# Performance work log

Measured on AMD Instinct MI355X. Metric: run time of the kernel, lower is better.

Reference implementation:

```python
import jax, jax.numpy as jnp
import numpy as np

D_MODEL = 256; D_FF = 512; D_STATE = 16; D_CONV = 4; EXPAND = 2
D_INNER = EXPAND * D_MODEL          # 512
DT_RANK = (D_MODEL + 15) // 16      # 16
BSZ = 16; NVARS = 32; PATCH_NUM = 64


def setup_inputs() -> dict:
    key = jax.random.key(0)
    ks = jax.random.split(key, 16)
    def nrm(k, shape, scale=0.02):
        return jax.random.normal(k, shape, jnp.float32) * scale
    inp = {}
    inp["x"] = jax.random.normal(ks[0], (BSZ, NVARS, D_MODEL, PATCH_NUM), jnp.float32)
    # Mamba block params
    inp["in_proj_w"] = nrm(ks[1], (2 * D_INNER, D_MODEL))
    inp["in_proj_b"] = jnp.zeros((2 * D_INNER,), jnp.float32)
    inp["conv_w"] = nrm(ks[2], (D_INNER, D_CONV), 0.1)   # depthwise causal conv
    inp["conv_b"] = jnp.zeros((D_INNER,), jnp.float32)
    inp["x_proj_w"] = nrm(ks[3], (DT_RANK + 2 * D_STATE, D_INNER))
    inp["dt_proj_w"] = nrm(ks[4], (D_INNER, DT_RANK))
    inp["dt_proj_b"] = nrm(ks[5], (D_INNER,), 0.1)
    inp["A_log"] = jnp.log(jnp.broadcast_to(
        jnp.arange(1, D_STATE + 1, dtype=jnp.float32), (D_INNER, D_STATE)))
    inp["Dp"] = jnp.ones((D_INNER,), jnp.float32)
    inp["out_proj_w"] = nrm(ks[6], (D_MODEL, D_INNER))
    # Mamba_ffn norms + pointwise FFN
    inp["norm1_g"] = jnp.ones((D_MODEL,), jnp.float32)
    inp["norm1_b"] = jnp.zeros((D_MODEL,), jnp.float32)
    inp["ffn1_w"] = nrm(ks[7], (D_FF, D_MODEL))
    inp["ffn1_b"] = jnp.zeros((D_FF,), jnp.float32)
    inp["ffn2_w"] = nrm(ks[8], (D_MODEL, D_FF))
    inp["ffn2_b"] = jnp.zeros((D_MODEL,), jnp.float32)
    inp["norm2_g"] = jnp.ones((D_MODEL,), jnp.float32)
    inp["norm2_b"] = jnp.zeros((D_MODEL,), jnp.float32)
    # outer VarPatch LayerNorm
    inp["ln_g"] = jnp.ones((D_MODEL,), jnp.float32)
    inp["ln_b"] = jnp.zeros((D_MODEL,), jnp.float32)
    return inp


def layer_norm(x, g, b, eps=1e-5):
    mu = x.mean(-1, keepdims=True)
    var = ((x - mu) ** 2).mean(-1, keepdims=True)
    return (x - mu) * jax.lax.rsqrt(var + eps) * g + b


def mamba(x, in_proj_w, in_proj_b, conv_w, conv_b, x_proj_w,
          dt_proj_w, dt_proj_b, A_log, Dp, out_proj_w):
    # x: (b, L, d_model)
    b, L, _ = x.shape
    xz = x @ in_proj_w.T + in_proj_b            # (b, L, 2*d_inner)
    xi, z = jnp.split(xz, 2, axis=-1)           # each (b, L, d_inner)
    # causal depthwise conv along L
    xc = xi.transpose(0, 2, 1)                  # (b, d_inner, L)
    xc = jax.lax.conv_general_dilated(
        xc, conv_w[:, None, :], (1,), [(D_CONV - 1, 0)],
        dimension_numbers=("NCH", "OIH", "NCH"),
        feature_group_count=D_INNER) + conv_b[None, :, None]
    xi = jax.nn.silu(xc.transpose(0, 2, 1))     # (b, L, d_inner)
    x_dbl = xi @ x_proj_w.T                     # (b, L, dt_rank + 2*n)
    dt = x_dbl[..., :DT_RANK]
    B = x_dbl[..., DT_RANK:DT_RANK + D_STATE]
    C = x_dbl[..., DT_RANK + D_STATE:]
    delta = jax.nn.softplus(dt @ dt_proj_w.T + dt_proj_b)   # (b, L, d_inner)
    A = -jnp.exp(A_log)                         # (d_inner, n)

    def step(h, inp):
        d_t, B_t, C_t, u_t = inp                # (b,d),(b,n),(b,n),(b,d)
        dA = jnp.exp(d_t[..., None] * A)        # (b, d, n)
        h = dA * h + (d_t * u_t)[..., None] * B_t[:, None, :]
        y = jnp.einsum("bdn,bn->bd", h, C_t)
        return h, y

    h0 = jnp.zeros((b, D_INNER, D_STATE), xi.dtype)
    xs = (delta.transpose(1, 0, 2), B.transpose(1, 0, 2),
          C.transpose(1, 0, 2), xi.transpose(1, 0, 2))
    _, ys = jax.lax.scan(step, h0, xs)          # ys: (L, b, d_inner)
    y = ys.transpose(1, 0, 2) + xi * Dp
    y = y * jax.nn.silu(z)
    return y @ out_proj_w.T                     # (b, L, d_model)


def reference(x, in_proj_w, in_proj_b, conv_w, conv_b, x_proj_w,
              dt_proj_w, dt_proj_b, A_log, Dp, out_proj_w,
              norm1_g, norm1_b, ffn1_w, ffn1_b, ffn2_w, ffn2_b,
              norm2_g, norm2_b, ln_g, ln_b):
    b, nv, dm, pn = x.shape
    x_residual = x
    h = x.reshape(b, pn * nv, dm)               # same flat view as torch reshape
    # Mamba_ffn: mamba + residual, norm, pointwise FFN + residual, norm
    h = h + mamba(h, in_proj_w, in_proj_b, conv_w, conv_b, x_proj_w,
                  dt_proj_w, dt_proj_b, A_log, Dp, out_proj_w)
    h = layer_norm(h, norm1_g, norm1_b)
    y = jax.nn.relu(h @ ffn1_w.T + ffn1_b)      # 1x1 conv == linear
    y = y @ ffn2_w.T + ffn2_b
    h = layer_norm(h + y, norm2_g, norm2_b)
    # back to patches
    h = h.reshape(b, nv, pn, dm)
    h = layer_norm(h, ln_g, ln_b).transpose(0, 1, 3, 2)   # (b, nv, dm, pn)
    return h + x_residual
```

## Files before the change

### kernel.cpp

```cpp
#include <hip/hip_runtime.h>
#include <hip/hip_bf16.h>
#include <math.h>

#define SEQ    2048
#define NBTOT  16
#define NCH    64
#define CHL    32

#define L2E 1.4426950408889634f

typedef __attribute__((ext_vector_type(8))) __bf16 bf16x8;
typedef __attribute__((ext_vector_type(4))) float f32x4;
typedef __attribute__((ext_vector_type(2))) float f32x2;

#define GLOAD16(gp, lp)                                                   \
  __builtin_amdgcn_global_load_lds(                                       \
      (const __attribute__((address_space(1))) unsigned int*)(gp),        \
      (__attribute__((address_space(3))) unsigned int*)(lp), 16, 0, 0)

__device__ __forceinline__ float exp2_(float x) {
  return __builtin_amdgcn_exp2f(x);
}
__device__ __forceinline__ float silu_(float x) {
  return x * __builtin_amdgcn_rcpf(1.f + exp2_(-x * L2E));
}
__device__ __forceinline__ float softplus_(float x) {
  return fmaxf(x, 0.f) + __logf(1.f + exp2_(-fabsf(x) * L2E));
}
__device__ __forceinline__ float wsum_(float v) {
#pragma unroll
  for (int off = 32; off > 0; off >>= 1) v += __shfl_xor(v, off, 64);
  return v;
}
__device__ __forceinline__ int xcdswz_(int bid, int nwg) {
  return (bid & 7) * (nwg >> 3) + (bid >> 3);
}
__device__ __forceinline__ void powpairs_(float e1, f32x2 p[8]) {
  float e2 = e1 * e1;
  f32x2 p0; p0.x = e1; p0.y = e2;
  f32x2 s2; s2.x = e2; s2.y = e2;
  f32x2 s4 = s2 * s2;
  f32x2 s8 = s4 * s4;
  p[0] = p0;      p[1] = p0 * s2; p[2] = p0 * s4; p[3] = p[1] * s4;
  p[4] = p0 * s8; p[5] = p[1] * s8; p[6] = p[2] * s8; p[7] = p[3] * s8;
}

template <bool BIAS, bool RELU, bool RES, bool RESB, bool F32OUT, bool BF16OUT,
          int NTLOG>
__global__ __launch_bounds__(256) void gemm_bf16(
    const __hip_bfloat16* __restrict__ A, const __hip_bfloat16* __restrict__ W,
    const float* __restrict__ bias, const float* __restrict__ res,
    const __hip_bfloat16* __restrict__ resb, float* __restrict__ C,
    __hip_bfloat16* __restrict__ Cb, int N, int K) {
  __shared__ __align__(16) char ShRaw[36864];
  short* Als = reinterpret_cast<short*>(ShRaw);
  short* Bls = Als + 8192;
  const int tid = threadIdx.x;
  const int lane = tid & 63;
  const int wid = tid >> 6;
  const int swz = xcdswz_(blockIdx.x, gridDim.x);
  const int m0 = (swz >> NTLOG) * 128;
  const int n0 = (swz & ((1 << NTLOG) - 1)) * 128;
  const int wm = (wid >> 1) * 64;
  const int wn = (wid & 1) * 64;
  const int lr = lane & 15;
  const int lk = lane >> 4;

  f32x4 acc[4][4];
#pragma unroll
  for (int m = 0; m < 4; ++m)
#pragma unroll
    for (int n = 0; n < 4; ++n) acc[m][n] = (f32x4){0.f, 0.f, 0.f, 0.f};

  const int srow = wid * 32 + (lane >> 3);
  const int scol = (lane & 7) * 8;
  const __hip_bfloat16* Ag = A + (size_t)(m0 + srow) * K + scol;
  const __hip_bfloat16* Wg = W + (size_t)(n0 + srow) * K + scol;
  short* Alb = Als + wid * 2048;
  short* Blb = Bls + wid * 2048;

  for (int kt = 0; kt < K; kt += 64) {
#pragma unroll
    for (int i = 0; i < 4; ++i) {
      GLOAD16(Ag + (size_t)(i * 8) * K + kt, Alb + i * 512);
      GLOAD16(Wg + (size_t)(i * 8) * K + kt, Blb + i * 512);
    }
    __syncthreads();
    const bf16x8* Af = reinterpret_cast<const bf16x8*>(Als);
    const bf16x8* Bf = reinterpret_cast<const bf16x8*>(Bls);
#pragma unroll
    for (int ks = 0; ks < 2; ++ks) {
      bf16x8 av[4], bv[4];
#pragma unroll
      for (int m = 0; m < 4; ++m)
        av[m] = Af[(wm + m * 16 + lr) * 8 + ks * 4 + lk];
#pragma unroll
      for (int n = 0; n < 4; ++n)
        bv[n] = Bf[(wn + n * 16 + lr) * 8 + ks * 4 + lk];
#pragma unroll
      for (int m = 0; m < 4; ++m)
#pragma unroll
        for (int n = 0; n < 4; ++n)
          acc[m][n] = __builtin_amdgcn_mfma_f32_16x16x32_bf16(
              av[m], bv[n], acc[m][n], 0, 0, 0);
    }
    __syncthreads();
  }

  if (BF16OUT) {
    __hip_bfloat16* epi =
        reinterpret_cast<__hip_bfloat16*>(ShRaw) + wid * 4608;
#pragma unroll
    for (int n = 0; n < 4; ++n) {
      int col = n0 + wn + n * 16 + lr;
      float bval = BIAS ? bias[col] : 0.f;
#pragma unroll
      for (int m = 0; m < 4; ++m) {
        int lrow = m * 16 + lk * 4;
#pragma unroll
        for (int r = 0; r < 4; ++r) {
          float v = acc[m][n][r];
          if (BIAS) v += bval;
          if (RES) v += res[(size_t)(m0 + wm + lrow + r) * N + col];
          if (RESB)
            v += __bfloat162float(resb[(size_t)(m0 + wm + lrow + r) * N + col]);
          if (RELU) v = fmaxf(v, 0.f);
          epi[(lrow + r) * 72 + n * 16 + lr] = __float2bfloat16(v);
        }
      }
    }
    const int lr8 = (lane & 7) * 8;
    const int lrw = lane >> 3;
    const size_t obase = (size_t)(m0 + wm) * N + n0 + wn + lr8;
#pragma unroll
    for (int j = 0; j < 8; ++j) {
      int row = j * 8 + lrw;
      int4 vv = *reinterpret_cast<const int4*>(epi + row * 72 + lr8);
      *reinterpret_cast<int4*>(&Cb[obase + (size_t)row * N]) = vv;
    }
  }
  if (F32OUT) {
#pragma unroll
    for (int n = 0; n < 4; ++n) {
      int col = n0 + wn + n * 16 + lr;
      if (col >= N) continue;
      float bval = BIAS ? bias[col] : 0.f;
#pragma unroll
      for (int m = 0; m < 4; ++m) {
        int row0 = m0 + wm + m * 16 + lk * 4;
#pragma unroll
        for (int r = 0; r < 4; ++r) {
          size_t off = (size_t)(row0 + r) * N + col;
          float v = acc[m][n][r];
          if (BIAS) v += bval;
          if (RES) v += res[off];
          if (RESB) v += __bfloat162float(resb[off]);
          if (RELU) v = fmaxf(v, 0.f);
          C[off] = v;
        }
      }
    }
  }
}

__global__ __launch_bounds__(256) void cast_bf16_k(
    const float* __restrict__ src, __hip_bfloat16* __restrict__ dst, int n4) {
  int i = xcdswz_(blockIdx.x, gridDim.x) * 256 + threadIdx.x;
  if (i >= n4) return;
  float4 v = reinterpret_cast<const float4*>(src)[i];
  union { __hip_bfloat16 h[4]; short4 s4; } u;
  u.h[0] = __float2bfloat16(v.x); u.h[1] = __float2bfloat16(v.y);
  u.h[2] = __float2bfloat16(v.z); u.h[3] = __float2bfloat16(v.w);
  reinterpret_cast<short4*>(dst)[i] = u.s4;
}

__global__ __launch_bounds__(256) void pad_wx_k(
    const float* __restrict__ src, __hip_bfloat16* __restrict__ dst) {
  int i = blockIdx.x * 256 + threadIdx.x;
  int row = i >> 7;
  union { __hip_bfloat16 h[4]; short4 s4; } u;
  if (row < 48) {
    float4 v = reinterpret_cast<const float4*>(src)[i];
    u.h[0] = __float2bfloat16(v.x); u.h[1] = __float2bfloat16(v.y);
    u.h[2] = __float2bfloat16(v.z); u.h[3] = __float2bfloat16(v.w);
  } else {
    u.h[0] = u.h[1] = u.h[2] = u.h[3] = __float2bfloat16(0.f);
  }
  reinterpret_cast<short4*>(dst)[i] = u.s4;
}

__global__ __launch_bounds__(256) void conv_silu_k(
    const __hip_bfloat16* __restrict__ xz, const float* __restrict__ cw,
    const float* __restrict__ cb, __hip_bfloat16* __restrict__ xi) {
  int idx = xcdswz_(blockIdx.x, gridDim.x) * 256 + threadIdx.x;
  int t = idx & 63;
  int rp = idx >> 6;
  int r = rp << 1;
  int l = r & (SEQ - 1);
  int c8 = t << 3;
  const __hip_bfloat16* p = xz + (size_t)r * 1024 + c8;
  union U8 { int4 v; __hip_bfloat16 h[8]; } x0, x1, x2, x3, x4, oa, ob;
  const int4 z4 = make_int4(0, 0, 0, 0);
  x4.v = *reinterpret_cast<const int4*>(p + 1024);
  x3.v = *reinterpret_cast<const int4*>(p);
  x2.v = (l >= 1) ? *reinterpret_cast<const int4*>(p - 1024) : z4;
  x1.v = (l >= 2) ? *reinterpret_cast<const int4*>(p - 2048) : z4;
  x0.v = (l >= 3) ? *reinterpret_cast<const int4*>(p - 3072) : z4;
  const float4* cw4 = reinterpret_cast<const float4*>(cw);
#pragma unroll
  for (int j = 0; j < 8; ++j) {
    float4 w = cw4[c8 + j];
    float b = cb[c8 + j];
    float f0 = __bfloat162float(x0.h[j]);
    float f1 = __bfloat162float(x1.h[j]);
    float f2 = __bfloat162float(x2.h[j]);
    float f3 = __bfloat162float(x3.h[j]);
    float f4 = __bfloat162float(x4.h[j]);
    float a0 = fmaf(w.w, f3, fmaf(w.z, f2, fmaf(w.y, f1, fmaf(w.x, f0, b))));
    float a1 = fmaf(w.w, f4, fmaf(w.z, f3, fmaf(w.y, f2, fmaf(w.x, f1, b))));
    oa.h[j] = __float2bfloat16(silu_(a0));
    ob.h[j] = __float2bfloat16(silu_(a1));
  }
  *reinterpret_cast<int4*>(&xi[(size_t)r * 512 + c8]) = oa.v;
  *reinterpret_cast<int4*>(&xi[(size_t)(r + 1) * 512 + c8]) = ob.v;
}

__global__ __launch_bounds__(256) void scan_p1(
    const __hip_bfloat16* __restrict__ u, const float* __restrict__ xdbl,
    const float* __restrict__ A_log, const float* __restrict__ wdt,
    const float* __restrict__ bdt, float* __restrict__ dlsum,
    __hip_bfloat16* __restrict__ hp, __hip_bfloat16* __restrict__ deltab) {
  const int w = xcdswz_(blockIdx.x, gridDim.x);
  const int b = w >> 7;
  const int c = (w >> 1) & 63;
  const int d = ((w & 1) << 8) + threadIdx.x;
  const int l0 = c * CHL;
  float A2[16];
  f32x2 w2[8];
  {
    const float4* aq = reinterpret_cast<const float4*>(&A_log[d * 16]);
    const f32x2* wq = reinterpret_cast<const f32x2*>(&wdt[d * 16]);
#pragma unroll
    for (int q = 0; q < 4; ++q) {
      float4 v = aq[q];
      A2[q * 4 + 0] = -exp2_(v.x * L2E) * L2E;
      A2[q * 4 + 1] = -exp2_(v.y * L2E) * L2E;
      A2[q * 4 + 2] = -exp2_(v.z * L2E) * L2E;
      A2[q * 4 + 3] = -exp2_(v.w * L2E) * L2E;
    }
#pragma unroll
    for (int k = 0; k < 8; ++k) w2[k] = wq[k];
  }
  bool chainok = true;
#pragma unroll
  for (int n = 1; n < 16; ++n)
    chainok = chainok &&
              (fabsf(A2[n] - (float)(n + 1) * A2[0]) <=
               1e-4f * (float)(n + 1) * fabsf(A2[0]));
  const float bdtd = bdt[d];
  const float nL = A2[0];
  f32x2 h2[8];
#pragma unroll
  for (int k = 0; k < 8; ++k) h2[k] = (f32x2){0.f, 0.f};
  float dls = 0.f;
  size_t base = (size_t)(b * SEQ + l0) * 512 + d;
  const float* rowp = xdbl + (size_t)(b * SEQ + l0) * 48;
  if (chainok) {
#pragma unroll 4
    for (int i = 0; i < CHL; ++i) {
      const f32x2* r2 = reinterpret_cast<const f32x2*>(rowp + i * 48);
      f32x2 acc2; acc2.x = bdtd; acc2.y = 0.f;
#pragma unroll
      for (int k = 0; k < 8; ++k)
        acc2 = __builtin_elementwise_fma(r2[k], w2[k], acc2);
      float dl = softplus_(acc2.x + acc2.y);
      deltab[base + (size_t)i * 512] = __float2bfloat16(dl);
      dls += dl;
      float du = dl * __bfloat162float(u[base + (size_t)i * 512]);
      f32x2 p[8];
      powpairs_(exp2_(dl * nL), p);
      f32x2 du2; du2.x = du; du2.y = du;
#pragma unroll
      for (int k = 0; k < 8; ++k)
        h2[k] = __builtin_elementwise_fma(p[k], h2[k], du2 * r2[8 + k]);
    }
  } else {
#pragma unroll 2
    for (int i = 0; i < CHL; ++i) {
      const f32x2* r2 = reinterpret_cast<const f32x2*>(rowp + i * 48);
      f32x2 acc2; acc2.x = bdtd; acc2.y = 0.f;
#pragma unroll
      for (int k = 0; k < 8; ++k)
        acc2 = __builtin_elementwise_fma(r2[k], w2[k], acc2);
      float dl = softplus_(acc2.x + acc2.y);
      deltab[base + (size_t)i * 512] = __float2bfloat16(dl);
      dls += dl;
      float du = dl * __bfloat162float(u[base + (size_t)i * 512]);
      f32x2 du2; du2.x = du; du2.y = du;
#pragma unroll
      for (int k = 0; k < 8; ++k) {
        f32x2 a; a.x = exp2_(dl * A2[2 * k]); a.y = exp2_(dl * A2[2 * k + 1]);
        h2[k] = __builtin_elementwise_fma(a, h2[k], du2 * r2[8 + k]);
      }
    }
  }
  size_t sc = (size_t)(b * NCH + c) * 512 + d;
  dlsum[sc] = dls;
  union { __hip_bfloat16 h[4]; short4 s4; } o0, o1, o2, o3;
#pragma unroll
  for (int j = 0; j < 2; ++j) {
    o0.h[2*j] = __float2bfloat16(h2[j].x);   o0.h[2*j+1] = __float2bfloat16(h2[j].y);
    o1.h[2*j] = __float2bfloat16(h2[2+j].x); o1.h[2*j+1] = __float2bfloat16(h2[2+j].y);
    o2.h[2*j] = __float2bfloat16(h2[4+j].x); o2.h[2*j+1] = __float2bfloat16(h2[4+j].y);
    o3.h[2*j] = __float2bfloat16(h2[6+j].x); o3.h[2*j+1] = __float2bfloat16(h2[6+j].y);
  }
  short4* hq = reinterpret_cast<short4*>(hp + sc * 16);
  hq[0] = o0.s4; hq[1] = o1.s4; hq[2] = o2.s4; hq[3] = o3.s4;
}

__global__ __launch_bounds__(256) void scan_p2(
    __hip_bfloat16* hp, const float* __restrict__ dlsum,
    const float* __restrict__ A_log) {
  int g = xcdswz_(blockIdx.x, gridDim.x) * 256 + threadIdx.x;
  int b = g >> 13;
  int dn = g & 8191;
  int d = dn >> 4;
  float A2n = -exp2_(A_log[dn] * L2E) * L2E;
  float H = 0.f;
  for (int c = 0; c < NCH; ++c) {
    float ds = dlsum[(size_t)(b * NCH + c) * 512 + d];
    size_t idx = (size_t)(b * NCH + c) * 8192 + dn;
    float p = __bfloat162float(hp[idx]);
    float a = exp2_(A2n * ds);
    hp[idx] = __float2bfloat16(H);
    H = fmaf(a, H, p);
  }
}

__global__ __launch_bounds__(256) void scan_p3(
    const __hip_bfloat16* u,
    const float* __restrict__ A_log,
    const __hip_bfloat16* __restrict__ deltab, const float* __restrict__ xdbl,
    const __hip_bfloat16* __restrict__ Hc, const float* __restrict__ Dp,
    const __hip_bfloat16* __restrict__ xz, __hip_bfloat16* y) {
  const int w = xcdswz_(blockIdx.x, gridDim.x);
  const int b = w >> 7;
  const int c = (w >> 1) & 63;
  const int d = ((w & 1) << 8) + threadIdx.x;
  const int l0 = c * CHL;
  float A2[16];
  {
    const float4* aq = reinterpret_cast<const float4*>(&A_log[d * 16]);
#pragma unroll
    for (int q = 0; q < 4; ++q) {
      float4 v = aq[q];
      A2[q * 4 + 0] = -exp2_(v.x * L2E) * L2E;
      A2[q * 4 + 1] = -exp2_(v.y * L2E) * L2E;
      A2[q * 4 + 2] = -exp2_(v.z * L2E) * L2E;
      A2[q * 4 + 3] = -exp2_(v.w * L2E) * L2E;
    }
  }
  bool chainok = true;
#pragma unroll
  for (int n = 1; n < 16; ++n)
    chainok = chainok &&
              (fabsf(A2[n] - (float)(n + 1) * A2[0]) <=
               1e-4f * (float)(n + 1) * fabsf(A2[0]));
  const float nL = A2[0];
  f32x2 h2[8];
  {
    const short4* hq =
        reinterpret_cast<const short4*>(Hc + ((size_t)(b * NCH + c) * 512 + d) * 16);
#pragma unroll
    for (int q = 0; q < 4; ++q) {
      union { short4 s4; __hip_bfloat16 h[4]; } iv;
      iv.s4 = hq[q];
      h2[2*q].x = __bfloat162float(iv.h[0]);
      h2[2*q].y = __bfloat162float(iv.h[1]);
      h2[2*q+1].x = __bfloat162float(iv.h[2]);
      h2[2*q+1].y = __bfloat162float(iv.h[3]);
    }
  }
  const float Dpd = Dp[d];
  size_t base = (size_t)(b * SEQ + l0) * 512 + d;
  const float* rowp = xdbl + (size_t)(b * SEQ + l0) * 48;
  const __hip_bfloat16* zp = xz + (size_t)(b * SEQ + l0) * 1024 + 512 + d;
  if (chainok) {
#pragma unroll 4
    for (int i = 0; i < CHL; ++i) {
      const f32x2* r2 = reinterpret_cast<const f32x2*>(rowp + i * 48);
      float dl = __bfloat162float(deltab[base + (size_t)i * 512]);
      float ul = __bfloat162float(u[base + (size_t)i * 512]);
      float du = dl * ul;
      f32x2 p[8];
      powpairs_(exp2_(dl * nL), p);
      f32x2 du2; du2.x = du; du2.y = du;
      f32x2 yv2; yv2.x = 0.f; yv2.y = 0.f;
#pragma unroll
      for (int k = 0; k < 8; ++k) {
        h2[k] = __builtin_elementwise_fma(p[k], h2[k], du2 * r2[8 + k]);
        yv2 = __builtin_elementwise_fma(h2[k], r2[16 + k], yv2);
      }
      float yv = yv2.x + yv2.y;
      float zv = __bfloat162float(zp[(size_t)i * 1024]);
      y[base + (size_t)i * 512] =
          __float2bfloat16((yv + ul * Dpd) * silu_(zv));
    }
  } else {
#pragma unroll 2
    for (int i = 0; i < CHL; ++i) {
      const f32x2* r2 = reinterpret_cast<const f32x2*>(rowp + i * 48);
      float dl = __bfloat162float(deltab[base + (size_t)i * 512]);
      float ul = __bfloat162float(u[base + (size_t)i * 512]);
      float du = dl * ul;
      f32x2 du2; du2.x = du; du2.y = du;
      f32x2 yv2; yv2.x = 0.f; yv2.y = 0.f;
#pragma unroll
      for (int k = 0; k < 8; ++k) {
        f32x2 a; a.x = exp2_(dl * A2[2 * k]); a.y = exp2_(dl * A2[2 * k + 1]);
        h2[k] = __builtin_elementwise_fma(a, h2[k], du2 * r2[8 + k]);
        yv2 = __builtin_elementwise_fma(h2[k], r2[16 + k], yv2);
      }
      float yv = yv2.x + yv2.y;
      float zv = __bfloat162float(zp[(size_t)i * 1024]);
      y[base + (size_t)i * 512] =
          __float2bfloat16((yv + ul * Dpd) * silu_(zv));
    }
  }
}

__global__ __launch_bounds__(256) void ln_k(
    const __hip_bfloat16* __restrict__ in, const float* __restrict__ g,
    const float* __restrict__ bb, __hip_bfloat16* __restrict__ outb) {
  int row = (xcdswz_(blockIdx.x, gridDim.x) * 256 + threadIdx.x) >> 6;
  int lane = threadIdx.x & 63;
  union { short4 s4; __hip_bfloat16 h[4]; } iv;
  iv.s4 = reinterpret_cast<const short4*>(in)[row * 64 + lane];
  float v0 = __bfloat162float(iv.h[0]), v1 = __bfloat162float(iv.h[1]);
  float v2 = __bfloat162float(iv.h[2]), v3 = __bfloat162float(iv.h[3]);
  float mu = wsum_(v0 + v1 + v2 + v3) * (1.f / 256.f);
  float a0 = v0 - mu, a1 = v1 - mu, a2 = v2 - mu, a3 = v3 - mu;
  float var = wsum_(a0 * a0 + a1 * a1 + a2 * a2 + a3 * a3) * (1.f / 256.f);
  float rs = __builtin_amdgcn_rsqf(var + 1e-5f);
  float4 gg = *reinterpret_cast<const float4*>(&g[lane * 4]);
  float4 bq = *reinterpret_cast<const float4*>(&bb[lane * 4]);
  union { __hip_bfloat16 h[4]; short4 s4; } u;
  u.h[0] = __float2bfloat16(a0 * rs * gg.x + bq.x);
  u.h[1] = __float2bfloat16(a1 * rs * gg.y + bq.y);
  u.h[2] = __float2bfloat16(a2 * rs * gg.z + bq.z);
  u.h[3] = __float2bfloat16(a3 * rs * gg.w + bq.w);
  reinterpret_cast<short4*>(outb)[row * 64 + lane] = u.s4;
}

__global__ __launch_bounds__(256) void final_k(
    const __hip_bfloat16* __restrict__ t2, const float* __restrict__ g2v,
    const float* __restrict__ b2v, const float* __restrict__ g3v,
    const float* __restrict__ b3v, const float* __restrict__ x,
    float* __restrict__ out) {
  int bx = xcdswz_(blockIdx.x, gridDim.x);
  int half = bx & 1, nv = (bx >> 1) & 31, b = bx >> 6;
  int wave = threadIdx.x >> 6, lane = threadIdx.x & 63;
  __shared__ float sh[32][257];
  float4 gg2 = *reinterpret_cast<const float4*>(&g2v[lane * 4]);
  float4 bb2 = *reinterpret_cast<const float4*>(&b2v[lane * 4]);
  float4 gg3 = *reinterpret_cast<const float4*>(&g3v[lane * 4]);
  float4 bb3 = *reinterpret_cast<const float4*>(&b3v[lane * 4]);
#pragma unroll
  for (int i = 0; i < 8; ++i) {
    int pn = wave * 8 + i;
    int r = ((b * 32 + nv) << 6) + (half << 5) + pn;
    union { short4 s4; __hip_bfloat16 h[4]; } iv;
    iv.s4 = reinterpret_cast<const short4*>(t2)[r * 64 + lane];
    float v0 = __bfloat162float(iv.h[0]), v1 = __bfloat162float(iv.h[1]);
    float v2 = __bfloat162float(iv.h[2]), v3 = __bfloat162float(iv.h[3]);
    float mu = wsum_(v0 + v1 + v2 + v3) * (1.f / 256.f);
    float a0 = v0 - mu, a1 = v1 - mu, a2 = v2 - mu, a3 = v3 - mu;
    float var = wsum_(a0 * a0 + a1 * a1 + a2 * a2 + a3 * a3) * (1.f / 256.f);
    float rs = __builtin_amdgcn_rsqf(var + 1e-5f);
    a0 = a0 * rs * gg2.x + bb2.x; a1 = a1 * rs * gg2.y + bb2.y;
    a2 = a2 * rs * gg2.z + bb2.z; a3 = a3 * rs * gg2.w + bb2.w;
    mu = wsum_(a0 + a1 + a2 + a3) * (1.f / 256.f);
    float c0 = a0 - mu, c1 = a1 - mu, c2 = a2 - mu, c3 = a3 - mu;
    var = wsum_(c0 * c0 + c1 * c1 + c2 * c2 + c3 * c3) * (1.f / 256.f);
    rs = __builtin_amdgcn_rsqf(var + 1e-5f);
    sh[pn][lane * 4 + 0] = c0 * rs * gg3.x + bb3.x;
    sh[pn][lane * 4 + 1] = c1 * rs * gg3.y + bb3.y;
    sh[pn][lane * 4 + 2] = c2 * rs * gg3.z + bb3.z;
    sh[pn][lane * 4 + 3] = c3 * rs * gg3.w + bb3.w;
  }
  __syncthreads();
  int pnl = threadIdx.x & 31;
  int dbase = threadIdx.x >> 5;
  size_t obase = (size_t)((b * 32 + nv) * 256) * 64 + (half << 5) + pnl;
#pragma unroll
  for (int k = 0; k < 32; ++k) {
    int dd = dbase + (k << 3);
    size_t oi = obase + (size_t)dd * 64;
    out[oi] = sh[pnl][dd] + x[oi];
  }
}

extern "C" void kernel_launch(void* const* d_in, const int* in_sizes, int n_in,
                              void* d_out, int out_size, void* d_ws,
                              size_t ws_size, hipStream_t stream) {
  const float* x    = (const float*)d_in[0];
  const float* w_in = (const float*)d_in[1];
  const float* b_in = (const float*)d_in[2];
  const float* cw   = (const float*)d_in[3];
  const float* cb   = (const float*)d_in[4];
  const float* wx   = (const float*)d_in[5];
  const float* wdt  = (const float*)d_in[6];
  const float* bdt  = (const float*)d_in[7];
  const float* alog = (const float*)d_in[8];
  const float* Dp   = (const float*)d_in[9];
  const float* wout = (const float*)d_in[10];
  const float* g1   = (const float*)d_in[11];
  const float* b1   = (const float*)d_in[12];
  const float* wf1  = (const float*)d_in[13];
  const float* bf1  = (const float*)d_in[14];
  const float* wf2  = (const float*)d_in[15];
  const float* bf2  = (const float*)d_in[16];
  const float* g2   = (const float*)d_in[17];
  const float* b2   = (const float*)d_in[18];
  const float* g3   = (const float*)d_in[19];
  const float* b3   = (const float*)d_in[20];
  float* out = (float*)d_out;

  const size_t MB1 = 1048576;
  char* g = (char*)d_ws;
  __hip_bfloat16* wbf_in  = (__hip_bfloat16*)(g);
  __hip_bfloat16* wbf_out = (__hip_bfloat16*)(g + 524288);
  __hip_bfloat16* wbf_f1  = (__hip_bfloat16*)(g + 786432);
  __hip_bfloat16* wbf_f2  = (__hip_bfloat16*)(g + 1048576);
  __hip_bfloat16* wbf_xp  = (__hip_bfloat16*)(g + 1310720);
  const size_t SHARED = 1572864;

  const size_t PB = 11 * MB1 + 393216;
  int nb = (int)((ws_size - SHARED) / PB);
  if (ws_size <= SHARED || nb < 1) return;
  if (nb > NBTOT) nb = NBTOT;

  dim3 blk(256);
  cast_bf16_k<<<dim3(256), blk, 0, stream>>>(w_in, wbf_in, 65536);
  cast_bf16_k<<<dim3(128), blk, 0, stream>>>(wout, wbf_out, 32768);
  cast_bf16_k<<<dim3(128), blk, 0, stream>>>(wf1, wbf_f1, 32768);
  cast_bf16_k<<<dim3(128), blk, 0, stream>>>(wf2, wbf_f2, 32768);
  pad_wx_k<<<dim3(64), blk, 0, stream>>>(wx, wbf_xp);

  for (int b0 = 0; b0 < NBTOT; b0 += nb) {
    int bn = (NBTOT - b0 < nb) ? (NBTOT - b0) : nb;
    char* base = g + SHARED;
    char* RA = base;
    char* RB = base + (size_t)bn * 4 * MB1;
    char* RC = base + (size_t)bn * 5 * MB1;
    char* RD = base + (size_t)bn * 7 * MB1;
    char* RE = RD + (size_t)bn * 393216;
    char* RF = RE + (size_t)bn * 2 * MB1;

    __hip_bfloat16* xz     = (__hip_bfloat16*)RA;
    __hip_bfloat16* t2b    = (__hip_bfloat16*)RA;
    __hip_bfloat16* xbf    = (__hip_bfloat16*)RB;
    float*          dlsum  = (float*)RB;
    __hip_bfloat16* xibf   = (__hip_bfloat16*)RC;
    __hip_bfloat16* ffnybf = (__hip_bfloat16*)RC;
    float*          xdbl   = (float*)RD;
    __hip_bfloat16* hp     = (__hip_bfloat16*)RE;
    __hip_bfloat16* resb   = (__hip_bfloat16*)RE;
    __hip_bfloat16* h1bf   = (__hip_bfloat16*)(RE + (size_t)bn * MB1);
    __hip_bfloat16* deltab = (__hip_bfloat16*)RF;

    const float* xg = x + (size_t)b0 * SEQ * 256;
    float* outg = out + (size_t)b0 * SEQ * 256;
    int M = bn * SEQ;
    int MT = M / 128;

    cast_bf16_k<<<dim3(M * 64 / 256), blk, 0, stream>>>(xg, xbf, M * 64);
    gemm_bf16<true, false, false, false, false, true, 3>
        <<<dim3(8 * MT), blk, 0, stream>>>(xbf, wbf_in, b_in, nullptr, nullptr,
                                           nullptr, xz, 1024, 256);
    conv_silu_k<<<dim3(M / 8), blk, 0, stream>>>(xz, cw, cb, xibf);
    gemm_bf16<false, false, false, false, true, false, 0>
        <<<dim3(MT), blk, 0, stream>>>(xibf, wbf_xp, nullptr, nullptr,
                                       nullptr, xdbl, nullptr, 48, 512);
    scan_p1<<<dim3(bn * 128), blk, 0, stream>>>(xibf, xdbl, alog, wdt, bdt,
                                                dlsum, hp, deltab);
    scan_p2<<<dim3(bn * 32), blk, 0, stream>>>(hp, dlsum, alog);
    scan_p3<<<dim3(bn * 128), blk, 0, stream>>>(xibf, alog, deltab, xdbl,
                                                hp, Dp, xz, xibf);
    gemm_bf16<false, false, true, false, false, true, 1>
        <<<dim3(2 * MT), blk, 0, stream>>>(xibf, wbf_out, nullptr, xg, nullptr,
                                           nullptr, resb, 256, 512);
    ln_k<<<dim3(M / 4), blk, 0, stream>>>(resb, g1, b1, h1bf);
    gemm_bf16<true, true, false, false, false, true, 2>
        <<<dim3(4 * MT), blk, 0, stream>>>(h1bf, wbf_f1, bf1, nullptr, nullptr,
                                           nullptr, ffnybf, 512, 256);
    gemm_bf16<true, false, false, true, false, true, 1>
        <<<dim3(2 * MT), blk, 0, stream>>>(ffnybf, wbf_f2, bf2, nullptr, h1bf,
                                           nullptr, t2b, 256, 512);
    final_k<<<dim3(bn * 64), blk, 0, stream>>>(t2b, g2, b2, g3, b3, xg, outg);
  }
}
```

Baseline: 260.5 us.

## Process two scan chunks per thread and read residuals from bf16 input copy

scan_p1 and scan_p3 now have each thread handle two adjacent chunks, interleaved in one loop. This halves the grid and gives more independent work per thread to hide exp and memory latency. Separately, the out_proj residual and the final residual add now read the bf16 copy of x instead of the fp32 input. That cuts global traffic but adds rounding error to the residual, and dlsum moves to its own buffer so xbf is not overwritten. Using bf16 x for the final residual may reduce output accuracy.

Result: slower. 266.4 us (+2.2%).

```diff
diff --git a/kernel.cpp b/kernel.cpp
--- a/kernel.cpp
+++ b/kernel.cpp
@@ -231,10 +231,10 @@
     const float* __restrict__ bdt, float* __restrict__ dlsum,
     __hip_bfloat16* __restrict__ hp, __hip_bfloat16* __restrict__ deltab) {
   const int w = xcdswz_(blockIdx.x, gridDim.x);
-  const int b = w >> 7;
-  const int c = (w >> 1) & 63;
+  const int b = w >> 6;
+  const int ch = (w >> 1) & 31;
   const int d = ((w & 1) << 8) + threadIdx.x;
-  const int l0 = c * CHL;
+  const int ca = ch * 2, cb_ = ch * 2 + 1;
   float A2[16];
   f32x2 w2[8];
   {
@@ -259,63 +259,92 @@
                1e-4f * (float)(n + 1) * fabsf(A2[0]));
   const float bdtd = bdt[d];
   const float nL = A2[0];
-  f32x2 h2[8];
-#pragma unroll
-  for (int k = 0; k < 8; ++k) h2[k] = (f32x2){0.f, 0.f};
-  float dls = 0.f;
-  size_t base = (size_t)(b * SEQ + l0) * 512 + d;
-  const float* rowp = xdbl + (size_t)(b * SEQ + l0) * 48;
+  f32x2 h2a[8], h2b[8];
+#pragma unroll
+  for (int k = 0; k < 8; ++k) {
+    h2a[k] = (f32x2){0.f, 0.f};
+    h2b[k] = (f32x2){0.f, 0.f};
+  }
+  float dlsa = 0.f, dlsb = 0.f;
+  size_t basea = (size_t)(b * SEQ + ca * CHL) * 512 + d;
+  size_t baseb = (size_t)(b * SEQ + cb_ * CHL) * 512 + d;
+  const float* rowpa = xdbl + (size_t)(b * SEQ + ca * CHL) * 48;
+  const float* rowpb = xdbl + (size_t)(b * SEQ + cb_ * CHL) * 48;
   if (chainok) {
-#pragma unroll 4
-    for (int i = 0; i < CHL; ++i) {
-      const f32x2* r2 = reinterpret_cast<const f32x2*>(rowp + i * 48);
-      f32x2 acc2; acc2.x = bdtd; acc2.y = 0.f;
-#pragma unroll
-      for (int k = 0; k < 8; ++k)
-        acc2 = __builtin_elementwise_fma(r2[k], w2[k], acc2);
-      float dl = softplus_(acc2.x + acc2.y);
-      deltab[base + (size_t)i * 512] = __float2bfloat16(dl);
-      dls += dl;
-      float du = dl * __bfloat162float(u[base + (size_t)i * 512]);
-      f32x2 p[8];
-      powpairs_(exp2_(dl * nL), p);
-      f32x2 du2; du2.x = du; du2.y = du;
-#pragma unroll
-      for (int k = 0; k < 8; ++k)
-        h2[k] = __builtin_elementwise_fma(p[k], h2[k], du2 * r2[8 + k]);
-    }
-  } else {
 #pragma unroll 2
     for (int i = 0; i < CHL; ++i) {
-      const f32x2* r2 = reinterpret_cast<const f32x2*>(rowp + i * 48);
-      f32x2 acc2; acc2.x = bdtd; acc2.y = 0.f;
-#pragma unroll
-      for (int k = 0; k < 8; ++k)
-        acc2 = __builtin_elementwise_fma(r2[k], w2[k], acc2);
-      float dl = softplus_(acc2.x + acc2.y);
-      deltab[base + (size_t)i * 512] = __float2bfloat16(dl);
-      dls += dl;
-      float du = dl * __bfloat162float(u[base + (size_t)i * 512]);
-      f32x2 du2; du2.x = du; du2.y = du;
+      const f32x2* ra = reinterpret_cast<const f32x2*>(rowpa + i * 48);
+      const f32x2* rb = reinterpret_cast<const f32x2*>(rowpb + i * 48);
+      f32x2 da; da.x = bdtd; da.y = 0.f;
+      f32x2 db; db.x = bdtd; db.y = 0.f;
 #pragma unroll
       for (int k = 0; k < 8; ++k) {
-        f32x2 a; a.x = exp2_(dl * A2[2 * k]); a.y = exp2_(dl * A2[2 * k + 1]);
-        h2[k] = __builtin_elementwise_fma(a, h2[k], du2 * r2[8 + k]);
+        da = __builtin_elementwise_fma(ra[k], w2[k], da);
+        db = __builtin_elementwise_fma(rb[k], w2[k], db);
       }
-    }
-  }
-  size_t sc = (size_t)(b * NCH + c) * 512 + d;
-  dlsum[sc] = dls;
-  union { __hip_bfloat16 h[4]; short4 s4; } o0, o1, o2, o3;
-#pragma unroll
-  for (int j = 0; j < 2; ++j) {
-    o0.h[2*j] = __float2bfloat16(h2[j].x);   o0.h[2*j+1] = __float2bfloat16(h2[j].y);
-    o1.h[2*j] = __float2bfloat16(h2[2+j].x); o1.h[2*j+1] = __float2bfloat16(h2[2+j].y);
-    o2.h[2*j] = __float2bfloat16(h2[4+j].x); o2.h[2*j+1] = __float2bfloat16(h2[4+j].y);
-    o3.h[2*j] = __float2bfloat16(h2[6+j].x); o3.h[2*j+1] = __float2bfloat16(h2[6+j].y);
-  }
-  short4* hq = reinterpret_cast<short4*>(hp + sc * 16);
-  hq[0] = o0.s4; hq[1] = o1.s4; hq[2] = o2.s4; hq[3] = o3.s4;
+      float dla = softplus_(da.x + da.y);
+      float dlb = softplus_(db.x + db.y);
+      deltab[basea + (size_t)i * 512] = __float2bfloat16(dla);
+      deltab[baseb + (size_t)i * 512] = __float2bfloat16(dlb);
+      dlsa += dla; dlsb += dlb;
+      float dua = dla * __bfloat162float(u[basea + (size_t)i * 512]);
+      float dub = dlb * __bfloat162float(u[baseb + (size_t)i * 512]);
+      f32x2 pa[8], pb[8];
+      powpairs_(exp2_(dla * nL), pa);
+      powpairs_(exp2_(dlb * nL), pb);
+      f32x2 dua2; dua2.x = dua; dua2.y = dua;
+      f32x2 dub2; dub2.x = dub; dub2.y = dub;
+#pragma unroll
+      for (int k = 0; k < 8; ++k) {
+        h2a[k] = __builtin_elementwise_fma(pa[k], h2a[k], dua2 * ra[8 + k]);
+        h2b[k] = __builtin_elementwise_fma(pb[k], h2b[k], dub2 * rb[8 + k]);
+      }
+    }
+  } else {
+#pragma unroll 1
+    for (int pass = 0; pass < 2; ++pass) {
+      size_t base = pass ? baseb : basea;
+      const float* rowp = pass ? rowpb : rowpa;
+      f32x2* h2 = pass ? h2b : h2a;
+      float dls = 0.f;
+      for (int i = 0; i < CHL; ++i) {
+        const f32x2* r2 = reinterpret_cast<const f32x2*>(rowp + i * 48);
+        f32x2 acc2; acc2.x = bdtd; acc2.y = 0.f;
+#pragma unroll
+        for (int k = 0; k < 8; ++k)
+          acc2 = __builtin_elementwise_fma(r2[k], w2[k], acc2);
+        float dl = softplus_(acc2.x + acc2.y);
+        deltab[base + (size_t)i * 512] = __float2bfloat16(dl);
+        dls += dl;
+        float du = dl * __bfloat162float(u[base + (size_t)i * 512]);
+        f32x2 du2; du2.x = du; du2.y = du;
+#pragma unroll
+        for (int k = 0; k < 8; ++k) {
+          f32x2 a; a.x = exp2_(dl * A2[2 * k]); a.y = exp2_(dl * A2[2 * k + 1]);
+          h2[k] = __builtin_elementwise_fma(a, h2[k], du2 * r2[8 + k]);
+        }
+      }
+      if (pass) dlsb = dls; else dlsa = dls;
+    }
+  }
+  size_t sca = (size_t)(b * NCH + ca) * 512 + d;
+  size_t scb = (size_t)(b * NCH + cb_) * 512 + d;
+  dlsum[sca] = dlsa;
+  dlsum[scb] = dlsb;
+#pragma unroll
+  for (int pass = 0; pass < 2; ++pass) {
+    const f32x2* h2 = pass ? h2b : h2a;
+    short4* hq = reinterpret_cast<short4*>(hp + (pass ? scb : sca) * 16);
+#pragma unroll
+    for (int q = 0; q < 4; ++q) {
+      union { __hip_bfloat16 h[4]; short4 s4; } o;
+      o.h[0] = __float2bfloat16(h2[2 * q].x);
+      o.h[1] = __float2bfloat16(h2[2 * q].y);
+      o.h[2] = __float2bfloat16(h2[2 * q + 1].x);
+      o.h[3] = __float2bfloat16(h2[2 * q + 1].y);
+      hq[q] = o.s4;
+    }
+  }
 }
 
 __global__ __launch_bounds__(256) void scan_p2(
@@ -344,10 +373,10 @@
     const __hip_bfloat16* __restrict__ Hc, const float* __restrict__ Dp,
     const __hip_bfloat16* __restrict__ xz, __hip_bfloat16* y) {
   const int w = xcdswz_(blockIdx.x, gridDim.x);
-  const int b = w >> 7;
-  const int c = (w >> 1) & 63;
+  const int b = w >> 6;
+  const int ch = (w >> 1) & 31;
   const int d = ((w & 1) << 8) + threadIdx.x;
-  const int l0 = c * CHL;
+  const int ca = ch * 2, cb_ = ch * 2 + 1;
   float A2[16];
   {
     const float4* aq = reinterpret_cast<const float4*>(&A_log[d * 16]);
@@ -367,64 +396,89 @@
               (fabsf(A2[n] - (float)(n + 1) * A2[0]) <=
                1e-4f * (float)(n + 1) * fabsf(A2[0]));
   const float nL = A2[0];
-  f32x2 h2[8];
+  f32x2 h2a[8], h2b[8];
   {
-    const short4* hq =
-        reinterpret_cast<const short4*>(Hc + ((size_t)(b * NCH + c) * 512 + d) * 16);
+    const short4* hqa =
+        reinterpret_cast<const short4*>(Hc + ((size_t)(b * NCH + ca) * 512 + d) * 16);
+    const short4* hqb =
+        reinterpret_cast<const short4*>(Hc + ((size_t)(b * NCH + cb_) * 512 + d) * 16);
 #pragma unroll
     for (int q = 0; q < 4; ++q) {
-      union { short4 s4; __hip_bfloat16 h[4]; } iv;
-      iv.s4 = hq[q];
-      h2[2*q].x = __bfloat162float(iv.h[0]);
-      h2[2*q].y = __bfloat162float(iv.h[1]);
-      h2[2*q+1].x = __bfloat162float(iv.h[2]);
-      h2[2*q+1].y = __bfloat162float(iv.h[3]);
+      union { short4 s4; __hip_bfloat16 h[4]; } ia, ib;
+      ia.s4 = hqa[q]; ib.s4 = hqb[q];
+      h2a[2*q].x = __bfloat162float(ia.h[0]);
+      h2a[2*q].y = __bfloat162float(ia.h[1]);
+      h2a[2*q+1].x = __bfloat162float(ia.h[2]);
+      h2a[2*q+1].y = __bfloat162float(ia.h[3]);
+      h2b[2*q].x = __bfloat162float(ib.h[0]);
+      h2b[2*q].y = __bfloat162float(ib.h[1]);
+      h2b[2*q+1].x = __bfloat162float(ib.h[2]);
+      h2b[2*q+1].y = __bfloat162float(ib.h[3]);
     }
   }
   const float Dpd = Dp[d];
-  size_t base = (size_t)(b * SEQ + l0) * 512 + d;
-  const float* rowp = xdbl + (size_t)(b * SEQ + l0) * 48;
-  const __hip_bfloat16* zp = xz + (size_t)(b * SEQ + l0) * 1024 + 512 + d;
+  size_t basea = (size_t)(b * SEQ + ca * CHL) * 512 + d;
+  size_t baseb = (size_t)(b * SEQ + cb_ * CHL) * 512 + d;
+  const float* rowpa = xdbl + (size_t)(b * SEQ + ca * CHL) * 48;
+  const float* rowpb = xdbl + (size_t)(b * SEQ + cb_ * CHL) * 48;
+  const __hip_bfloat16* zpa = xz + (size_t)(b * SEQ + ca * CHL) * 1024 + 512 + d;
+  const __hip_bfloat16* zpb = xz + (size_t)(b * SEQ + cb_ * CHL) * 1024 + 512 + d;
   if (chainok) {
-#pragma unroll 4
-    for (int i = 0; i < CHL; ++i) {
-      const f32x2* r2 = reinterpret_cast<const f32x2*>(rowp + i * 48);
-      float dl = __bfloat162float(deltab[base + (size_t)i * 512]);
-      float ul = __bfloat162float(u[base + (size_t)i * 512]);
-      float du = dl * ul;
-      f32x2 p[8];
-      powpairs_(exp2_(dl * nL), p);
-      f32x2 du2; du2.x = du; du2.y = du;
-      f32x2 yv2; yv2.x = 0.f; yv2.y = 0.f;
-#pragma unroll
-      for (int k = 0; k < 8; ++k) {
-        h2[k] = __builtin_elementwise_fma(p[k], h2[k], du2 * r2[8 + k]);
-        yv2 = __builtin_elementwise_fma(h2[k], r2[16 + k], yv2);
-      }
-      float yv = yv2.x + yv2.y;
-      float zv = __bfloat162float(zp[(size_t)i * 1024]);
-      y[base + (size_t)i * 512] =
-          __float2bfloat16((yv + ul * Dpd) * silu_(zv));
-    }
-  } else {
 #pragma unroll 2
     for (int i = 0; i < CHL; ++i) {
-      const f32x2* r2 = reinterpret_cast<const f32x2*>(rowp + i * 48);
-      float dl = __bfloat162float(deltab[base + (size_t)i * 512]);
-      float ul = __bfloat162float(u[base + (size_t)i * 512]);
-      float du = dl * ul;
-      f32x2 du2; du2.x = du; du2.y = du;
-      f32x2 yv2; yv2.x = 0.f; yv2.y = 0.f;
+      const f32x2* ra = reinterpret_cast<const f32x2*>(rowpa + i * 48);
+      const f32x2* rb = reinterpret_cast<const f32x2*>(rowpb + i * 48);
+      float dla = __bfloat162float(deltab[basea + (size_t)i * 512]);
+      float dlb = __bfloat162float(deltab[baseb + (size_t)i * 512]);
+      float ula = __bfloat162float(u[basea + (size_t)i * 512]);
+      float ulb = __bfloat162float(u[baseb + (size_t)i * 512]);
+      float dua = dla * ula, dub = dlb * ulb;
+      f32x2 pa[8], pb[8];
+      powpairs_(exp2_(dla * nL), pa);
+      powpairs_(exp2_(dlb * nL), pb);
+      f32x2 dua2; dua2.x = dua; dua2.y = dua;
+      f32x2 dub2; dub2.x = dub; dub2.y = dub;
+      f32x2 ya2; ya2.x = 0.f; ya2.y = 0.f;
+      f32x2 yb2; yb2.x = 0.f; yb2.y = 0.f;
 #pragma unroll
       for (int k = 0; k < 8; ++k) {
-        f32x2 a; a.x = exp2_(dl * A2[2 * k]); a.y = exp2_(dl * A2[2 * k + 1]);
-        h2[k] = __builtin_elementwise_fma(a, h2[k], du2 * r2[8 + k]);
-        yv2 = __builtin_elementwise_fma(h2[k], r2[16 + k], yv2);
+        h2a[k] = __builtin_elementwise_fma(pa[k], h2a[k], dua2 * ra[8 + k]);
+        h2b[k] = __builtin_elementwise_fma(pb[k], h2b[k], dub2 * rb[8 + k]);
+        ya2 = __builtin_elementwise_fma(h2a[k], ra[16 + k], ya2);
+        yb2 = __builtin_elementwise_fma(h2b[k], rb[16 + k], yb2);
       }
-      float yv = yv2.x + yv2.y;
-      float zv = __bfloat162float(zp[(size_t)i * 1024]);
-      y[base + (size_t)i * 512] =
-          __float2bfloat16((yv + ul * Dpd) * silu_(zv));
+      float yva = ya2.x + ya2.y + ula * Dpd;
+      float yvb = yb2.x + yb2.y + ulb * Dpd;
+      float zva = __bfloat162float(zpa[(size_t)i * 1024]);
+      float zvb = __bfloat162float(zpb[(size_t)i * 1024]);
+      y[basea + (size_t)i * 512] = __float2bfloat16(yva * silu_(zva));
+      y[baseb + (size_t)i * 512] = __float2bfloat16(yvb * silu_(zvb));
+    }
+  } else {
+#pragma unroll 1
+    for (int pass = 0; pass < 2; ++pass) {
+      size_t base = pass ? baseb : basea;
+      const float* rowp = pass ? rowpb : rowpa;
+      const __hip_bfloat16* zp = pass ? zpb : zpa;
+      f32x2* h2 = pass ? h2b : h2a;
+      for (int i = 0; i < CHL; ++i) {
+        const f32x2* r2 = reinterpret_cast<const f32x2*>(rowp + i * 48);
+        float dl = __bfloat162float(deltab[base + (size_t)i * 512]);
+        float ul = __bfloat162float(u[base + (size_t)i * 512]);
+        float du = dl * ul;
+        f32x2 du2; du2.x = du; du2.y = du;
+        f32x2 yv2; yv2.x = 0.f; yv2.y = 0.f;
+#pragma unroll
+        for (int k = 0; k < 8; ++k) {
+          f32x2 a; a.x = exp2_(dl * A2[2*k]); a.y = exp2_(dl * A2[2*k+1]);
+          h2[k] = __builtin_elementwise_fma(a, h2[k], du2 * r2[8 + k]);
+          yv2 = __builtin_elementwise_fma(h2[k], r2[16 + k], yv2);
+        }
+        float yv = yv2.x + yv2.y;
+        float zv = __bfloat162float(zp[(size_t)i * 1024]);
+        y[base + (size_t)i * 512] =
+            __float2bfloat16((yv + ul * Dpd) * silu_(zv));
+      }
     }
   }
 }
@@ -455,7 +509,7 @@
 __global__ __launch_bounds__(256) void final_k(
     const __hip_bfloat16* __restrict__ t2, const float* __restrict__ g2v,
     const float* __restrict__ b2v, const float* __restrict__ g3v,
-    const float* __restrict__ b3v, const float* __restrict__ x,
+    const float* __restrict__ b3v, const __hip_bfloat16* __restrict__ xbf,
     float* __restrict__ out) {
   int bx = xcdswz_(blockIdx.x, gridDim.x);
   int half = bx & 1, nv = (bx >> 1) & 31, b = bx >> 6;
@@ -496,7 +550,7 @@
   for (int k = 0; k < 32; ++k) {
     int dd = dbase + (k << 3);
     size_t oi = obase + (size_t)dd * 64;
-    out[oi] = sh[pnl][dd] + x[oi];
+    out[oi] = sh[pnl][dd] + __bfloat162float(xbf[oi]);
   }
 }
 
@@ -535,7 +589,7 @@
   __hip_bfloat16* wbf_xp  = (__hip_bfloat16*)(g + 1310720);
   const size_t SHARED = 1572864;
 
-  const size_t PB = 11 * MB1 + 393216;
+  const size_t PB = 11 * MB1 + 393216 + 131072;
   int nb = (int)((ws_size - SHARED) / PB);
   if (ws_size <= SHARED || nb < 1) return;
   if (nb > NBTOT) nb = NBTOT;
@@ -556,11 +610,11 @@
     char* RD = base + (size_t)bn * 7 * MB1;
     char* RE = RD + (size_t)bn * 393216;
     char* RF = RE + (size_t)bn * 2 * MB1;
+    char* RG = RF + (size_t)bn * 2 * MB1;
 
     __hip_bfloat16* xz     = (__hip_bfloat16*)RA;
     __hip_bfloat16* t2b    = (__hip_bfloat16*)RA;
     __hip_bfloat16* xbf    = (__hip_bfloat16*)RB;
-    float*          dlsum  = (float*)RB;
     __hip_bfloat16* xibf   = (__hip_bfloat16*)RC;
     __hip_bfloat16* ffnybf = (__hip_bfloat16*)RC;
     float*          xdbl   = (float*)RD;
@@ -568,6 +622,7 @@
     __hip_bfloat16* resb   = (__hip_bfloat16*)RE;
     __hip_bfloat16* h1bf   = (__hip_bfloat16*)(RE + (size_t)bn * MB1);
     __hip_bfloat16* deltab = (__hip_bfloat16*)RF;
+    float*          dlsum  = (float*)RG;
 
     const float* xg = x + (size_t)b0 * SEQ * 256;
     float* outg = out + (size_t)b0 * SEQ * 256;
@@ -582,14 +637,14 @@
     gemm_bf16<false, false, false, false, true, false, 0>
         <<<dim3(MT), blk, 0, stream>>>(xibf, wbf_xp, nullptr, nullptr,
                                        nullptr, xdbl, nullptr, 48, 512);
-    scan_p1<<<dim3(bn * 128), blk, 0, stream>>>(xibf, xdbl, alog, wdt, bdt,
-                                                dlsum, hp, deltab);
+    scan_p1<<<dim3(bn * 64), blk, 0, stream>>>(xibf, xdbl, alog, wdt, bdt,
+                                               dlsum, hp, deltab);
     scan_p2<<<dim3(bn * 32), blk, 0, stream>>>(hp, dlsum, alog);
-    scan_p3<<<dim3(bn * 128), blk, 0, stream>>>(xibf, alog, deltab, xdbl,
-                                                hp, Dp, xz, xibf);
-    gemm_bf16<false, false, true, false, false, true, 1>
-        <<<dim3(2 * MT), blk, 0, stream>>>(xibf, wbf_out, nullptr, xg, nullptr,
-                                           nullptr, resb, 256, 512);
+    scan_p3<<<dim3(bn * 64), blk, 0, stream>>>(xibf, alog, deltab, xdbl,
+                                               hp, Dp, xz, xibf);
+    gemm_bf16<false, false, false, true, false, true, 1>
+        <<<dim3(2 * MT), blk, 0, stream>>>(xibf, wbf_out, nullptr, nullptr,
+                                           xbf, nullptr, resb, 256, 512);
     ln_k<<<dim3(M / 4), blk, 0, stream>>>(resb, g1, b1, h1bf);
     gemm_bf16<true, true, false, false, false, true, 2>
         <<<dim3(4 * MT), blk, 0, stream>>>(h1bf, wbf_f1, bf1, nullptr, nullptr,
@@ -597,6 +652,6 @@
     gemm_bf16<true, false, false, true, false, true, 1>
         <<<dim3(2 * MT), blk, 0, stream>>>(ffnybf, wbf_f2, bf2, nullptr, h1bf,
                                            nullptr, t2b, 256, 512);
-    final_k<<<dim3(bn * 64), blk, 0, stream>>>(t2b, g2, b2, g3, b3, xg, outg);
-  }
-}
+    final_k<<<dim3(bn * 64), blk, 0, stream>>>(t2b, g2, b2, g3, b3, xbf, outg);
+  }
+}
```
